# Kernel optimization log

Hardware: AMD Instinct MI355X
Metric: run time of the kernel (lower is better)

The kernel has to match this reference:

```python
import jax, jax.numpy as jnp
import numpy as np

N = 20000      # nodes
E = 640000     # edges
D_IN = 128
D_OUT = 128
EPS_LN = 1e-6


def setup_inputs() -> dict:
    key = jax.random.key(0)
    ks = jax.random.split(key, 12)
    h = jax.random.normal(ks[0], (N, D_IN), dtype=jnp.float32)
    r = jax.random.normal(ks[1], (E, D_IN), dtype=jnp.float32)
    src = jax.random.randint(ks[2], (E,), 0, N, dtype=jnp.int32)
    dst = jax.random.randint(ks[3], (E,), 0, N, dtype=jnp.int32)
    # LayerNorm params (head, tail, rel)
    hn_a = jnp.ones((D_IN,), jnp.float32); hn_b = jnp.zeros((D_IN,), jnp.float32)
    tn_a = jnp.ones((D_IN,), jnp.float32); tn_b = jnp.zeros((D_IN,), jnp.float32)
    rn_a = jnp.ones((D_IN,), jnp.float32); rn_b = jnp.zeros((D_IN,), jnp.float32)
    sc = 1.0 / np.sqrt(D_IN)
    head_w = jax.random.normal(ks[4], (D_IN,), jnp.float32) * sc
    tail_w = jax.random.normal(ks[5], (D_IN,), jnp.float32) * sc
    rel_w = jax.random.normal(ks[6], (D_IN,), jnp.float32) * sc
    fc_w = jax.random.normal(ks[7], (D_IN, D_OUT), jnp.float32) * sc
    fc_b = jnp.zeros((D_OUT,), jnp.float32)
    return {"h": h, "r": r, "src": src, "dst": dst,
            "hn_a": hn_a, "hn_b": hn_b, "tn_a": tn_a, "tn_b": tn_b,
            "rn_a": rn_a, "rn_b": rn_b,
            "head_w": head_w, "tail_w": tail_w, "rel_w": rel_w,
            "fc_w": fc_w, "fc_b": fc_b}


def _layer_norm(x, a, b):
    # faithful to torch: std with Bessel correction (unbiased), eps added to std
    mean = x.mean(axis=-1, keepdims=True)
    var = jnp.sum((x - mean) ** 2, axis=-1, keepdims=True) / (x.shape[-1] - 1)
    std = jnp.sqrt(var)
    return a * (x - mean) / (std + EPS_LN) + b


def reference(h, r, src, dst, hn_a, hn_b, tn_a, tn_b, rn_a, rn_b,
              head_w, tail_w, rel_w, fc_w, fc_b):
    # per-node / per-edge scalar attention logits
    eh = jnp.tanh(_layer_norm(h, hn_a, hn_b) @ head_w)   # [N]
    et = jnp.tanh(_layer_norm(h, tn_a, tn_b) @ tail_w)   # [N]
    er = jnp.tanh(_layer_norm(r, rn_a, rn_b) @ rel_w)    # [E]
    # edge attention: act(eh[src] + et[dst] + er), activation = relu
    e = jax.nn.relu(eh[src] + et[dst] + er)              # [E]
    # edge_softmax: softmax over incoming edges of each destination node
    emax = jax.ops.segment_max(e, dst, num_segments=N)   # [N]
    ex = jnp.exp(e - emax[dst])
    esum = jax.ops.segment_sum(ex, dst, num_segments=N)  # [N]
    a = ex / esum[dst]                                   # [E]
    # u_mul_e + sum aggregation: feat[v] = sum_{(u->v)} a_e * h[u]
    msg = h[src] * a[:, None]                            # [E, D_IN]
    feat = jax.ops.segment_sum(msg, dst, num_segments=N) # [N, D_IN]
    out = feat @ fc_w + fc_b                             # [N, D_OUT]
    # F.normalize(p=2, dim=1)
    nrm = jnp.sqrt(jnp.sum(out * out, axis=1, keepdims=True))
    return out / jnp.maximum(nrm, 1e-12)
```

## Files before the change

### kernel.cpp

```cpp
#include <hip/hip_runtime.h>
#include <stdint.h>

#define D_DIM 128
#define EPS_LN 1e-6f
#define NA 20480

__device__ __forceinline__ float tanh_fast(float x) {
    return 1.0f - 2.0f / (__expf(2.0f * x) + 1.0f);
}

__device__ __forceinline__ float wave_sum(float v) {
    #pragma unroll
    for (int m = 1; m < 64; m <<= 1) v += __shfl_xor(v, m, 64);
    return v;
}

__device__ __forceinline__ float group16_sum(float v) {
    #pragma unroll
    for (int m = 1; m < 16; m <<= 1) v += __shfl_xor(v, m, 64);
    return v;
}

__device__ __forceinline__ float dot8_ln(const float4& a, const float4& b,
                                         float mean, float inv,
                                         const float4& wa0, const float4& wa1,
                                         const float4& wb0, const float4& wb1,
                                         const float4& ww0, const float4& ww1) {
    float p = 0.0f;
    p += ((a.x - mean) * inv * wa0.x + wb0.x) * ww0.x;
    p += ((a.y - mean) * inv * wa0.y + wb0.y) * ww0.y;
    p += ((a.z - mean) * inv * wa0.z + wb0.z) * ww0.z;
    p += ((a.w - mean) * inv * wa0.w + wb0.w) * ww0.w;
    p += ((b.x - mean) * inv * wa1.x + wb1.x) * ww1.x;
    p += ((b.y - mean) * inv * wa1.y + wb1.y) * ww1.y;
    p += ((b.z - mean) * inv * wa1.z + wb1.z) * ww1.z;
    p += ((b.w - mean) * inv * wa1.w + wb1.w) * ww1.w;
    return p;
}

__global__ __launch_bounds__(256) void k_node(
    const float* __restrict__ h,
    const float* __restrict__ hn_a, const float* __restrict__ hn_b,
    const float* __restrict__ tn_a, const float* __restrict__ tn_b,
    const float* __restrict__ head_w, const float* __restrict__ tail_w,
    float* __restrict__ eh, float* __restrict__ et, int n)
{
    int gid  = blockIdx.x * 256 + threadIdx.x;
    int node = gid >> 4;
    int sub  = threadIdx.x & 15;
    if (node >= n) return;

    const float4* hp = (const float4*)(h + (size_t)node * 128);
    float4 a = hp[sub * 2], b = hp[sub * 2 + 1];

    float s  = a.x + a.y + a.z + a.w + b.x + b.y + b.z + b.w;
    float s2 = a.x*a.x + a.y*a.y + a.z*a.z + a.w*a.w
             + b.x*b.x + b.y*b.y + b.z*b.z + b.w*b.w;
    s  = group16_sum(s);
    s2 = group16_sum(s2);
    float mean = s * (1.0f / 128.0f);
    float var  = fmaxf((s2 - s * mean) * (1.0f / 127.0f), 0.0f);
    float inv  = 1.0f / (sqrtf(var) + EPS_LN);

    int i0 = sub * 2, i1 = sub * 2 + 1;
    float4 ha0 = ((const float4*)hn_a)[i0],  ha1 = ((const float4*)hn_a)[i1];
    float4 hb0 = ((const float4*)hn_b)[i0],  hb1 = ((const float4*)hn_b)[i1];
    float4 hw0 = ((const float4*)head_w)[i0],hw1 = ((const float4*)head_w)[i1];
    float4 ta0 = ((const float4*)tn_a)[i0],  ta1 = ((const float4*)tn_a)[i1];
    float4 tb0 = ((const float4*)tn_b)[i0],  tb1 = ((const float4*)tn_b)[i1];
    float4 tw0 = ((const float4*)tail_w)[i0],tw1 = ((const float4*)tail_w)[i1];

    float ph = dot8_ln(a, b, mean, inv, ha0, ha1, hb0, hb1, hw0, hw1);
    float pt = dot8_ln(a, b, mean, inv, ta0, ta1, tb0, tb1, tw0, tw1);
    ph = group16_sum(ph);
    pt = group16_sum(pt);

    if (sub == 0) {
        eh[node] = tanh_fast(ph);
        et[node] = tanh_fast(pt);
    }
}

__global__ __launch_bounds__(256) void k_histo(
    const int* __restrict__ dst, int* __restrict__ cnt, int nE)
{
    int e = blockIdx.x * 256 + threadIdx.x;
    if (e < nE) atomicAdd(cnt + dst[e], 1);
}

__global__ __launch_bounds__(256) void k_scanA(
    const int* __restrict__ cnt, int* __restrict__ offl,
    int* __restrict__ bsum, int n)
{
    __shared__ int sscan[4];
    int b = blockIdx.x;
    int i = (b << 8) + threadIdx.x;
    int v = (i < n) ? cnt[i] : 0;
    int lane = threadIdx.x & 63, w4 = threadIdx.x >> 6;
    int x = v;
    #pragma unroll
    for (int s = 1; s < 64; s <<= 1) {
        int t = __shfl_up(x, s, 64);
        if (lane >= s) x += t;
    }
    if (lane == 63) sscan[w4] = x;
    __syncthreads();
    if (threadIdx.x == 0) {
        int a0 = sscan[0], a1 = sscan[1], a2 = sscan[2], a3 = sscan[3];
        sscan[0] = 0; sscan[1] = a0; sscan[2] = a0 + a1; sscan[3] = a0 + a1 + a2;
        bsum[b] = a0 + a1 + a2 + a3;
    }
    __syncthreads();
    offl[i] = sscan[w4] + x - v;
}

__global__ __launch_bounds__(256) void k_scanB(
    const int* __restrict__ bsum, int* __restrict__ bpre, int nb)
{
    __shared__ int sscan[4];
    int t = threadIdx.x;
    int v = (t < nb) ? bsum[t] : 0;
    int lane = t & 63, w4 = t >> 6;
    int x = v;
    #pragma unroll
    for (int s = 1; s < 64; s <<= 1) {
        int tt = __shfl_up(x, s, 64);
        if (lane >= s) x += tt;
    }
    if (lane == 63) sscan[w4] = x;
    __syncthreads();
    if (t == 0) {
        int a0 = sscan[0], a1 = sscan[1], a2 = sscan[2], a3 = sscan[3];
        sscan[0] = 0; sscan[1] = a0; sscan[2] = a0 + a1; sscan[3] = a0 + a1 + a2;
    }
    __syncthreads();
    bpre[t] = sscan[w4] + x - v;
}

__global__ __launch_bounds__(256) void k_combine(
    const int* __restrict__ offl, const int* __restrict__ bpre,
    int* __restrict__ off, int n)
{
    int i = blockIdx.x * 256 + threadIdx.x;
    if (i <= n) off[i] = offl[i] + bpre[i >> 8];
}

__global__ __launch_bounds__(256) void k_edge(
    const float* __restrict__ r,
    const float* __restrict__ rn_a, const float* __restrict__ rn_b,
    const float* __restrict__ rel_w,
    const int* __restrict__ src, const int* __restrict__ dst,
    const float* __restrict__ eh, const float* __restrict__ et,
    const int* __restrict__ off, int* __restrict__ rankc,
    int2* __restrict__ edata, int nE)
{
    int gid  = blockIdx.x * 256 + threadIdx.x;
    int edge = gid >> 4;
    int sub  = threadIdx.x & 15;
    if (edge >= nE) return;

    int sN = 0, dN = 0, base = 0;
    float vh = 0.0f, vt = 0.0f;
    if (sub == 0) {
        sN = src[edge]; dN = dst[edge];
        vh = eh[sN];    vt = et[dN];
        base = off[dN];
    }

    const float4* rp = (const float4*)(r + (size_t)edge * 128);
    float4 a = rp[sub * 2], b = rp[sub * 2 + 1];

    float s  = a.x + a.y + a.z + a.w + b.x + b.y + b.z + b.w;
    float s2 = a.x*a.x + a.y*a.y + a.z*a.z + a.w*a.w
             + b.x*b.x + b.y*b.y + b.z*b.z + b.w*b.w;
    s  = group16_sum(s);
    s2 = group16_sum(s2);
    float mean = s * (1.0f / 128.0f);
    float var  = fmaxf((s2 - s * mean) * (1.0f / 127.0f), 0.0f);
    float inv  = 1.0f / (sqrtf(var) + EPS_LN);

    int i0 = sub * 2, i1 = sub * 2 + 1;
    float4 ra0 = ((const float4*)rn_a)[i0],  ra1 = ((const float4*)rn_a)[i1];
    float4 rb0 = ((const float4*)rn_b)[i0],  rb1 = ((const float4*)rn_b)[i1];
    float4 rw0 = ((const float4*)rel_w)[i0], rw1 = ((const float4*)rel_w)[i1];

    float pr = dot8_ln(a, b, mean, inv, ra0, ra1, rb0, rb1, rw0, rw1);
    pr = group16_sum(pr);

    if (sub == 0) {
        float v = tanh_fast(pr) + vh + vt;
        v = fmaxf(v, 0.0f);
        int rank = atomicAdd(rankc + dN, 1);
        edata[base + rank] = make_int2(sN, __float_as_int(__expf(v)));
    }
}

__global__ __launch_bounds__(256) void k_gather(
    const float* __restrict__ h,
    const int* __restrict__ off, const int2* __restrict__ edata,
    float* __restrict__ feat, int n)
{
    int wid = threadIdx.x >> 6, lane = threadIdx.x & 63;
    int v = blockIdx.x * 4 + wid;
    if (v >= n) return;

    int beg = off[v], end = off[v + 1];
    const float2* h2 = (const float2*)h;

    float acc0 = 0.0f, acc1 = 0.0f;
    float acc2 = 0.0f, acc3 = 0.0f;
    float ws0 = 0.0f, ws1 = 0.0f;

    for (int i = beg; i < end; i += 8) {
        int m = end - i;
        int2   q_[8];
        float2 p_[8];
        #pragma unroll
        for (int j = 0; j < 8; j++)
            if (j < m) q_[j] = edata[i + j];
        #pragma unroll
        for (int j = 0; j < 8; j++)
            if (j < m) p_[j] = h2[(size_t)q_[j].x * 64 + lane];
        #pragma unroll
        for (int j = 0; j < 8; j += 2) {
            if (j < m) {
                float w = __int_as_float(q_[j].y);
                acc0 += w * p_[j].x; acc1 += w * p_[j].y; ws0 += w;
            }
            if (j + 1 < m) {
                float w = __int_as_float(q_[j + 1].y);
                acc2 += w * p_[j + 1].x; acc3 += w * p_[j + 1].y; ws1 += w;
            }
        }
    }
    acc0 += acc2; acc1 += acc3;
    float wsum = ws0 + ws1;

    float inv = (end > beg) ? (1.0f / wsum) : 0.0f;
    float2 q; q.x = acc0 * inv; q.y = acc1 * inv;
    ((float2*)feat)[(size_t)v * 64 + lane] = q;
}

__global__ __launch_bounds__(256) void k_gemv(
    const float* __restrict__ feat,
    const float* __restrict__ fc_w, const float* __restrict__ fc_b,
    float* __restrict__ out, int n)
{
    __shared__ float wl[64][128];
    __shared__ float fl[16][128];
    int tid = threadIdx.x, lane = tid & 63, wid = tid >> 6;
    int vbase = blockIdx.x * 16;

    {
        const float4* fp = (const float4*)(feat + (size_t)vbase * 128);
        for (int k = tid; k < 512; k += 256) {
            int row = k >> 5;
            ((float4*)fl)[k] = (vbase + row < n) ? fp[k] : make_float4(0, 0, 0, 0);
        }
    }

    float o0[4], o1[4];
    float2 bb = ((const float2*)fc_b)[lane];
    #pragma unroll
    for (int t = 0; t < 4; t++) { o0[t] = bb.x; o1[t] = bb.y; }

    for (int half = 0; half < 2; half++) {
        __syncthreads();
        const float4* wp = (const float4*)(fc_w + half * 64 * 128);
        for (int k = tid; k < 2048; k += 256)
            ((float4*)wl)[k] = wp[k];
        __syncthreads();
        #pragma unroll 4
        for (int d = 0; d < 64; d++) {
            float2 ww = ((const float2*)(wl[d]))[lane];
            #pragma unroll
            for (int t = 0; t < 4; t++) {
                float f = fl[wid * 4 + t][half * 64 + d];
                o0[t] += f * ww.x;
                o1[t] += f * ww.y;
            }
        }
    }

    #pragma unroll
    for (int t = 0; t < 4; t++) {
        int v = vbase + wid * 4 + t;
        if (v >= n) continue;
        float nrm2 = wave_sum(o0[t] * o0[t] + o1[t] * o1[t]);
        float invn = 1.0f / fmaxf(sqrtf(nrm2), 1e-12f);
        float2 q; q.x = o0[t] * invn; q.y = o1[t] * invn;
        ((float2*)out)[(size_t)v * 64 + lane] = q;
    }
}

extern "C" void kernel_launch(void* const* d_in, const int* in_sizes, int n_in,
                              void* d_out, int out_size, void* d_ws, size_t ws_size,
                              hipStream_t stream)
{
    const float* h      = (const float*)d_in[0];
    const float* r      = (const float*)d_in[1];
    const int*   src    = (const int*)d_in[2];
    const int*   dst    = (const int*)d_in[3];
    const float* hn_a   = (const float*)d_in[4];
    const float* hn_b   = (const float*)d_in[5];
    const float* tn_a   = (const float*)d_in[6];
    const float* tn_b   = (const float*)d_in[7];
    const float* rn_a   = (const float*)d_in[8];
    const float* rn_b   = (const float*)d_in[9];
    const float* head_w = (const float*)d_in[10];
    const float* tail_w = (const float*)d_in[11];
    const float* rel_w  = (const float*)d_in[12];
    const float* fc_w   = (const float*)d_in[13];
    const float* fc_b   = (const float*)d_in[14];

    int N = in_sizes[0] / D_DIM;
    int E = in_sizes[2];

    float* base  = (float*)d_ws;
    float* eh    = base;
    float* et    = base + NA;
    int*   cnt   = (int*)(base + 2 * NA);
    int*   rankc = (int*)(base + 3 * NA);
    int*   offl  = (int*)(base + 4 * NA);
    int*   off   = (int*)(base + 5 * NA);
    int*   bsum  = (int*)(base + 6 * NA);
    int*   bpre  = bsum + 256;
    float* feat  = base + 6 * NA + 512;
    int2*  edata = (int2*)(feat + (size_t)NA * 128);

    hipMemsetAsync(cnt, 0, 2 * (size_t)NA * sizeof(int), stream);

    int B1 = (N + 256) >> 8;

    k_node<<<(N * 16 + 255) / 256, 256, 0, stream>>>(
        h, hn_a, hn_b, tn_a, tn_b, head_w, tail_w, eh, et, N);
    k_histo<<<(E + 255) / 256, 256, 0, stream>>>(dst, cnt, E);
    k_scanA<<<B1, 256, 0, stream>>>(cnt, offl, bsum, N);
    k_scanB<<<1, 256, 0, stream>>>(bsum, bpre, B1);
    k_combine<<<(N + 1 + 255) / 256, 256, 0, stream>>>(offl, bpre, off, N);
    k_edge<<<(E * 16 + 255) / 256, 256, 0, stream>>>(
        r, rn_a, rn_b, rel_w, src, dst, eh, et, off, rankc, edata, E);
    k_gather<<<(N + 3) / 4, 256, 0, stream>>>(h, off, edata, feat, N);
    k_gemv<<<(N + 15) / 16, 256, 0, stream>>>(feat, fc_w, fc_b, (float*)d_out, N);
}
```

Measured before the change: 590.6 us.

## Fuse histogram into node kernel, drop combine pass, widen gather loads

The destination histogram now runs as a grid-stride loop inside the node LayerNorm kernel, and the separate offset-combine kernel is gone. Consumers now rebuild offsets on the fly from the local scan plus the block prefix. The gather kernel splits each wave into two halves, each handling a different edge with float4 loads, then merges the halves with a cross-lane shuffle. This removes two launches and an offset buffer pass, at the cost of extra index arithmetic and a reduction step in the gather.

```diff
diff --git a/kernel.cpp b/kernel.cpp
--- a/kernel.cpp
+++ b/kernel.cpp
@@ -43,15 +43,123 @@
     const float* __restrict__ hn_a, const float* __restrict__ hn_b,
     const float* __restrict__ tn_a, const float* __restrict__ tn_b,
     const float* __restrict__ head_w, const float* __restrict__ tail_w,
-    float* __restrict__ eh, float* __restrict__ et, int n)
+    const int* __restrict__ dst, int* __restrict__ cnt,
+    float* __restrict__ eh, float* __restrict__ et, int n, int nE)
 {
     int gid  = blockIdx.x * 256 + threadIdx.x;
     int node = gid >> 4;
     int sub  = threadIdx.x & 15;
-    if (node >= n) return;
-
-    const float4* hp = (const float4*)(h + (size_t)node * 128);
-    float4 a = hp[sub * 2], b = hp[sub * 2 + 1];
+
+    if (node < n) {
+        const float4* hp = (const float4*)(h + (size_t)node * 128);
+        float4 a = hp[sub * 2], b = hp[sub * 2 + 1];
+
+        float s  = a.x + a.y + a.z + a.w + b.x + b.y + b.z + b.w;
+        float s2 = a.x*a.x + a.y*a.y + a.z*a.z + a.w*a.w
+                 + b.x*b.x + b.y*b.y + b.z*b.z + b.w*b.w;
+        s  = group16_sum(s);
+        s2 = group16_sum(s2);
+        float mean = s * (1.0f / 128.0f);
+        float var  = fmaxf((s2 - s * mean) * (1.0f / 127.0f), 0.0f);
+        float inv  = 1.0f / (sqrtf(var) + EPS_LN);
+
+        int i0 = sub * 2, i1 = sub * 2 + 1;
+        float4 ha0 = ((const float4*)hn_a)[i0],  ha1 = ((const float4*)hn_a)[i1];
+        float4 hb0 = ((const float4*)hn_b)[i0],  hb1 = ((const float4*)hn_b)[i1];
+        float4 hw0 = ((const float4*)head_w)[i0],hw1 = ((const float4*)head_w)[i1];
+        float4 ta0 = ((const float4*)tn_a)[i0],  ta1 = ((const float4*)tn_a)[i1];
+        float4 tb0 = ((const float4*)tn_b)[i0],  tb1 = ((const float4*)tn_b)[i1];
+        float4 tw0 = ((const float4*)tail_w)[i0],tw1 = ((const float4*)tail_w)[i1];
+
+        float ph = dot8_ln(a, b, mean, inv, ha0, ha1, hb0, hb1, hw0, hw1);
+        float pt = dot8_ln(a, b, mean, inv, ta0, ta1, tb0, tb1, tw0, tw1);
+        ph = group16_sum(ph);
+        pt = group16_sum(pt);
+
+        if (sub == 0) {
+            eh[node] = tanh_fast(ph);
+            et[node] = tanh_fast(pt);
+        }
+    }
+
+    int gthreads = gridDim.x * 256;
+    for (int e = gid; e < nE; e += gthreads)
+        atomicAdd(cnt + dst[e], 1);
+}
+
+__global__ __launch_bounds__(256) void k_scanA(
+    const int* __restrict__ cnt, int* __restrict__ offl,
+    int* __restrict__ bsum, int n)
+{
+    __shared__ int sscan[4];
+    int b = blockIdx.x;
+    int i = (b << 8) + threadIdx.x;
+    int v = (i < n) ? cnt[i] : 0;
+    int lane = threadIdx.x & 63, w4 = threadIdx.x >> 6;
+    int x = v;
+    #pragma unroll
+    for (int s = 1; s < 64; s <<= 1) {
+        int t = __shfl_up(x, s, 64);
+        if (lane >= s) x += t;
+    }
+    if (lane == 63) sscan[w4] = x;
+    __syncthreads();
+    if (threadIdx.x == 0) {
+        int a0 = sscan[0], a1 = sscan[1], a2 = sscan[2], a3 = sscan[3];
+        sscan[0] = 0; sscan[1] = a0; sscan[2] = a0 + a1; sscan[3] = a0 + a1 + a2;
+        bsum[b] = a0 + a1 + a2 + a3;
+    }
+    __syncthreads();
+    offl[i] = sscan[w4] + x - v;
+}
+
+__global__ __launch_bounds__(256) void k_scanB(
+    const int* __restrict__ bsum, int* __restrict__ bpre, int nb)
+{
+    __shared__ int sscan[4];
+    int t = threadIdx.x;
+    int v = (t < nb) ? bsum[t] : 0;
+    int lane = t & 63, w4 = t >> 6;
+    int x = v;
+    #pragma unroll
+    for (int s = 1; s < 64; s <<= 1) {
+        int tt = __shfl_up(x, s, 64);
+        if (lane >= s) x += tt;
+    }
+    if (lane == 63) sscan[w4] = x;
+    __syncthreads();
+    if (t == 0) {
+        int a0 = sscan[0], a1 = sscan[1], a2 = sscan[2], a3 = sscan[3];
+        sscan[0] = 0; sscan[1] = a0; sscan[2] = a0 + a1; sscan[3] = a0 + a1 + a2;
+    }
+    __syncthreads();
+    bpre[t] = sscan[w4] + x - v;
+}
+
+__global__ __launch_bounds__(256) void k_edge(
+    const float* __restrict__ r,
+    const float* __restrict__ rn_a, const float* __restrict__ rn_b,
+    const float* __restrict__ rel_w,
+    const int* __restrict__ src, const int* __restrict__ dst,
+    const float* __restrict__ eh, const float* __restrict__ et,
+    const int* __restrict__ offl, const int* __restrict__ bpre,
+    int* __restrict__ rankc, int2* __restrict__ edata, int nE)
+{
+    int gid  = blockIdx.x * 256 + threadIdx.x;
+    int edge = gid >> 4;
+    int sub  = threadIdx.x & 15;
+    if (edge >= nE) return;
+
+    int sN = 0, dN = 0, base = 0;
+    float vh = 0.0f, vt = 0.0f;
+    if (sub == 0) {
+        sN = src[edge]; dN = dst[edge];
+        vh = eh[sN];    vt = et[dN];
+        base = offl[dN] + bpre[dN >> 8];
+    }
+
+    const float4* rp = (const float4*)(r + (size_t)edge * 128);
+    float4 a = rp[sub * 2], b = rp[sub * 2 + 1];
 
     float s  = a.x + a.y + a.z + a.w + b.x + b.y + b.z + b.w;
     float s2 = a.x*a.x + a.y*a.y + a.z*a.z + a.w*a.w
@@ -63,123 +171,6 @@
     float inv  = 1.0f / (sqrtf(var) + EPS_LN);
 
     int i0 = sub * 2, i1 = sub * 2 + 1;
-    float4 ha0 = ((const float4*)hn_a)[i0],  ha1 = ((const float4*)hn_a)[i1];
-    float4 hb0 = ((const float4*)hn_b)[i0],  hb1 = ((const float4*)hn_b)[i1];
-    float4 hw0 = ((const float4*)head_w)[i0],hw1 = ((const float4*)head_w)[i1];
-    float4 ta0 = ((const float4*)tn_a)[i0],  ta1 = ((const float4*)tn_a)[i1];
-    float4 tb0 = ((const float4*)tn_b)[i0],  tb1 = ((const float4*)tn_b)[i1];
-    float4 tw0 = ((const float4*)tail_w)[i0],tw1 = ((const float4*)tail_w)[i1];
-
-    float ph = dot8_ln(a, b, mean, inv, ha0, ha1, hb0, hb1, hw0, hw1);
-    float pt = dot8_ln(a, b, mean, inv, ta0, ta1, tb0, tb1, tw0, tw1);
-    ph = group16_sum(ph);
-    pt = group16_sum(pt);
-
-    if (sub == 0) {
-        eh[node] = tanh_fast(ph);
-        et[node] = tanh_fast(pt);
-    }
-}
-
-__global__ __launch_bounds__(256) void k_histo(
-    const int* __restrict__ dst, int* __restrict__ cnt, int nE)
-{
-    int e = blockIdx.x * 256 + threadIdx.x;
-    if (e < nE) atomicAdd(cnt + dst[e], 1);
-}
-
-__global__ __launch_bounds__(256) void k_scanA(
-    const int* __restrict__ cnt, int* __restrict__ offl,
-    int* __restrict__ bsum, int n)
-{
-    __shared__ int sscan[4];
-    int b = blockIdx.x;
-    int i = (b << 8) + threadIdx.x;
-    int v = (i < n) ? cnt[i] : 0;
-    int lane = threadIdx.x & 63, w4 = threadIdx.x >> 6;
-    int x = v;
-    #pragma unroll
-    for (int s = 1; s < 64; s <<= 1) {
-        int t = __shfl_up(x, s, 64);
-        if (lane >= s) x += t;
-    }
-    if (lane == 63) sscan[w4] = x;
-    __syncthreads();
-    if (threadIdx.x == 0) {
-        int a0 = sscan[0], a1 = sscan[1], a2 = sscan[2], a3 = sscan[3];
-        sscan[0] = 0; sscan[1] = a0; sscan[2] = a0 + a1; sscan[3] = a0 + a1 + a2;
-        bsum[b] = a0 + a1 + a2 + a3;
-    }
-    __syncthreads();
-    offl[i] = sscan[w4] + x - v;
-}
-
-__global__ __launch_bounds__(256) void k_scanB(
-    const int* __restrict__ bsum, int* __restrict__ bpre, int nb)
-{
-    __shared__ int sscan[4];
-    int t = threadIdx.x;
-    int v = (t < nb) ? bsum[t] : 0;
-    int lane = t & 63, w4 = t >> 6;
-    int x = v;
-    #pragma unroll
-    for (int s = 1; s < 64; s <<= 1) {
-        int tt = __shfl_up(x, s, 64);
-        if (lane >= s) x += tt;
-    }
-    if (lane == 63) sscan[w4] = x;
-    __syncthreads();
-    if (t == 0) {
-        int a0 = sscan[0], a1 = sscan[1], a2 = sscan[2], a3 = sscan[3];
-        sscan[0] = 0; sscan[1] = a0; sscan[2] = a0 + a1; sscan[3] = a0 + a1 + a2;
-    }
-    __syncthreads();
-    bpre[t] = sscan[w4] + x - v;
-}
-
-__global__ __launch_bounds__(256) void k_combine(
-    const int* __restrict__ offl, const int* __restrict__ bpre,
-    int* __restrict__ off, int n)
-{
-    int i = blockIdx.x * 256 + threadIdx.x;
-    if (i <= n) off[i] = offl[i] + bpre[i >> 8];
-}
-
-__global__ __launch_bounds__(256) void k_edge(
-    const float* __restrict__ r,
-    const float* __restrict__ rn_a, const float* __restrict__ rn_b,
-    const float* __restrict__ rel_w,
-    const int* __restrict__ src, const int* __restrict__ dst,
-    const float* __restrict__ eh, const float* __restrict__ et,
-    const int* __restrict__ off, int* __restrict__ rankc,
-    int2* __restrict__ edata, int nE)
-{
-    int gid  = blockIdx.x * 256 + threadIdx.x;
-    int edge = gid >> 4;
-    int sub  = threadIdx.x & 15;
-    if (edge >= nE) return;
-
-    int sN = 0, dN = 0, base = 0;
-    float vh = 0.0f, vt = 0.0f;
-    if (sub == 0) {
-        sN = src[edge]; dN = dst[edge];
-        vh = eh[sN];    vt = et[dN];
-        base = off[dN];
-    }
-
-    const float4* rp = (const float4*)(r + (size_t)edge * 128);
-    float4 a = rp[sub * 2], b = rp[sub * 2 + 1];
-
-    float s  = a.x + a.y + a.z + a.w + b.x + b.y + b.z + b.w;
-    float s2 = a.x*a.x + a.y*a.y + a.z*a.z + a.w*a.w
-             + b.x*b.x + b.y*b.y + b.z*b.z + b.w*b.w;
-    s  = group16_sum(s);
-    s2 = group16_sum(s2);
-    float mean = s * (1.0f / 128.0f);
-    float var  = fmaxf((s2 - s * mean) * (1.0f / 127.0f), 0.0f);
-    float inv  = 1.0f / (sqrtf(var) + EPS_LN);
-
-    int i0 = sub * 2, i1 = sub * 2 + 1;
     float4 ra0 = ((const float4*)rn_a)[i0],  ra1 = ((const float4*)rn_a)[i1];
     float4 rb0 = ((const float4*)rn_b)[i0],  rb1 = ((const float4*)rn_b)[i1];
     float4 rw0 = ((const float4*)rel_w)[i0], rw1 = ((const float4*)rel_w)[i1];
@@ -197,48 +188,56 @@
 
 __global__ __launch_bounds__(256) void k_gather(
     const float* __restrict__ h,
-    const int* __restrict__ off, const int2* __restrict__ edata,
+    const int* __restrict__ offl, const int* __restrict__ bpre,
+    const int2* __restrict__ edata,
     float* __restrict__ feat, int n)
 {
     int wid = threadIdx.x >> 6, lane = threadIdx.x & 63;
     int v = blockIdx.x * 4 + wid;
     if (v >= n) return;
-
-    int beg = off[v], end = off[v + 1];
-    const float2* h2 = (const float2*)h;
-
-    float acc0 = 0.0f, acc1 = 0.0f;
-    float acc2 = 0.0f, acc3 = 0.0f;
-    float ws0 = 0.0f, ws1 = 0.0f;
+    int half = lane >> 5, l5 = lane & 31;
+
+    int beg = offl[v]     + bpre[v >> 8];
+    int end = offl[v + 1] + bpre[(v + 1) >> 8];
+
+    const float4* h4 = (const float4*)h;
+
+    float a0 = 0.0f, a1 = 0.0f, a2 = 0.0f, a3 = 0.0f, ws = 0.0f;
 
     for (int i = beg; i < end; i += 8) {
-        int m = end - i;
-        int2   q_[8];
-        float2 p_[8];
+        int2   q_[4];
+        float4 p_[4];
+        bool   ok_[4];
         #pragma unroll
-        for (int j = 0; j < 8; j++)
-            if (j < m) q_[j] = edata[i + j];
+        for (int pp = 0; pp < 4; pp++) {
+            int e = i + 2 * pp + half;
+            ok_[pp] = (e < end);
+            if (ok_[pp]) q_[pp] = edata[e];
+        }
         #pragma unroll
-        for (int j = 0; j < 8; j++)
-            if (j < m) p_[j] = h2[(size_t)q_[j].x * 64 + lane];
+        for (int pp = 0; pp < 4; pp++)
+            if (ok_[pp]) p_[pp] = h4[(size_t)q_[pp].x * 32 + l5];
         #pragma unroll
-        for (int j = 0; j < 8; j += 2) {
-            if (j < m) {
-                float w = __int_as_float(q_[j].y);
-                acc0 += w * p_[j].x; acc1 += w * p_[j].y; ws0 += w;
+        for (int pp = 0; pp < 4; pp++)
+            if (ok_[pp]) {
+                float w = __int_as_float(q_[pp].y);
+                a0 += w * p_[pp].x; a1 += w * p_[pp].y;
+                a2 += w * p_[pp].z; a3 += w * p_[pp].w;
+                ws += w;
             }
-            if (j + 1 < m) {
-                float w = __int_as_float(q_[j + 1].y);
-                acc2 += w * p_[j + 1].x; acc3 += w * p_[j + 1].y; ws1 += w;
-            }
-        }
-    }
-    acc0 += acc2; acc1 += acc3;
-    float wsum = ws0 + ws1;
-
-    float inv = (end > beg) ? (1.0f / wsum) : 0.0f;
-    float2 q; q.x = acc0 * inv; q.y = acc1 * inv;
-    ((float2*)feat)[(size_t)v * 64 + lane] = q;
+    }
+    a0 += __shfl_xor(a0, 32, 64);
+    a1 += __shfl_xor(a1, 32, 64);
+    a2 += __shfl_xor(a2, 32, 64);
+    a3 += __shfl_xor(a3, 32, 64);
+    ws += __shfl_xor(ws, 32, 64);
+
+    float inv = (end > beg) ? (1.0f / ws) : 0.0f;
+    if (half == 0) {
+        float4 qo;
+        qo.x = a0 * inv; qo.y = a1 * inv; qo.z = a2 * inv; qo.w = a3 * inv;
+        ((float4*)feat)[(size_t)v * 32 + l5] = qo;
+    }
 }
 
 __global__ __launch_bounds__(256) void k_gemv(
@@ -322,10 +321,9 @@
     int*   cnt   = (int*)(base + 2 * NA);
     int*   rankc = (int*)(base + 3 * NA);
     int*   offl  = (int*)(base + 4 * NA);
-    int*   off   = (int*)(base + 5 * NA);
-    int*   bsum  = (int*)(base + 6 * NA);
+    int*   bsum  = (int*)(base + 5 * NA);
     int*   bpre  = bsum + 256;
-    float* feat  = base + 6 * NA + 512;
+    float* feat  = base + 5 * NA + 512;
     int2*  edata = (int2*)(feat + (size_t)NA * 128);
 
     hipMemsetAsync(cnt, 0, 2 * (size_t)NA * sizeof(int), stream);
@@ -333,13 +331,11 @@
     int B1 = (N + 256) >> 8;
 
     k_node<<<(N * 16 + 255) / 256, 256, 0, stream>>>(
-        h, hn_a, hn_b, tn_a, tn_b, head_w, tail_w, eh, et, N);
-    k_histo<<<(E + 255) / 256, 256, 0, stream>>>(dst, cnt, E);
+        h, hn_a, hn_b, tn_a, tn_b, head_w, tail_w, dst, cnt, eh, et, N, E);
     k_scanA<<<B1, 256, 0, stream>>>(cnt, offl, bsum, N);
     k_scanB<<<1, 256, 0, stream>>>(bsum, bpre, B1);
-    k_combine<<<(N + 1 + 255) / 256, 256, 0, stream>>>(offl, bpre, off, N);
     k_edge<<<(E * 16 + 255) / 256, 256, 0, stream>>>(
-        r, rn_a, rn_b, rel_w, src, dst, eh, et, off, rankc, edata, E);
-    k_gather<<<(N + 3) / 4, 256, 0, stream>>>(h, off, edata, feat, N);
+        r, rn_a, rn_b, rel_w, src, dst, eh, et, offl, bpre, rankc, edata, E);
+    k_gather<<<(N + 3) / 4, 256, 0, stream>>>(h, offl, bpre, edata, feat, N);
     k_gemv<<<(N + 15) / 16, 256, 0, stream>>>(feat, fc_w, fc_b, (float*)d_out, N);
 }
```

Result: faster. 576.5 us (-2.4%).
